# Kernel optimization log

Measured on AMD Instinct MI355X. Metric: run time of the kernel, lower is better.

## Reference

```python
import jax, jax.numpy as jnp
import numpy as np

N = 50000
E = 524288
FA = 133
FB = 14
H = 128
DEPTH = 3


def setup_inputs() -> dict:
    key = jax.random.key(0)
    ks = jax.random.split(key, 8)
    atom_features = jax.random.normal(ks[0], (N, FA), dtype=jnp.float32)
    bond_features = jax.random.normal(ks[1], (E, FB), dtype=jnp.float32)
    edge_index = jax.random.randint(ks[2], (2, E), 0, N, dtype=jnp.int64)
    s_init = 1.0 / np.sqrt(FA + FB)
    s_upd = 1.0 / np.sqrt(2 * H)
    s_read = 1.0 / np.sqrt(H)
    W_init = jax.random.uniform(ks[3], (H, FA + FB), jnp.float32, -s_init, s_init)
    b_init = jnp.zeros((H,), jnp.float32)
    W_upd = jax.random.uniform(ks[4], (H, 2 * H), jnp.float32, -s_upd, s_upd)
    b_upd = jnp.zeros((H,), jnp.float32)
    W_read = jax.random.uniform(ks[5], (H, H), jnp.float32, -s_read, s_read)
    b_read = jnp.zeros((H,), jnp.float32)
    return {
        "atom_features": atom_features,
        "bond_features": bond_features,
        "edge_index": edge_index,
        "W_init": W_init, "b_init": b_init,
        "W_upd": W_upd, "b_upd": b_upd,
        "W_read": W_read, "b_read": b_read,
    }


def reference(atom_features, bond_features, edge_index,
              W_init, b_init, W_upd, b_upd, W_read, b_read):
    src = edge_index[0]
    dst = edge_index[1]
    # edge init: concat(atom[src], bond) -> linear -> relu   [E, H]
    init_in = jnp.concatenate([atom_features[src], bond_features], axis=-1)
    h = jax.nn.relu(init_in @ W_init.T + b_init)
    rev = jnp.arange(E, dtype=jnp.int64) ^ 1  # reverse-edge pairing
    for _ in range(DEPTH):
        sum_in = jax.ops.segment_sum(h, dst, num_segments=N)  # [N, H]
        m = sum_in[src] - h[rev]                              # [E, H]
        h = jax.nn.relu(jnp.concatenate([h, m], axis=-1) @ W_upd.T + b_upd)
    atom_embed = jax.ops.segment_sum(h, dst, num_segments=N)  # [N, H]
    atom_embed = jax.nn.relu(atom_embed @ W_read.T + b_read)
    return atom_embed.sum(axis=0)  # [H]
```

## Files before the change

### kernel.cpp

```cpp
#include <hip/hip_runtime.h>
#include <stdint.h>
#include <stddef.h>

#define N_ATOMS 50000
#define N_EDGES 524288
#define FA 133
#define FB 14
#define H 128
#define DEPTH 3
#define KI 160
#define KB 32
#define KR 128
#define SCAN_NB 98

typedef __attribute__((ext_vector_type(8))) __bf16 bf16x8;
typedef __attribute__((ext_vector_type(4))) float f32x4;

__device__ __forceinline__ uint16_t f2bf(float f) {
    uint32_t u = __builtin_bit_cast(uint32_t, f);
    return (uint16_t)((u + 0x7FFFu + ((u >> 16) & 1u)) >> 16);
}
__device__ __forceinline__ float bf2f(uint16_t h) {
    return __builtin_bit_cast(float, (uint32_t)h << 16);
}

__device__ __forceinline__ void async_load16(const uint16_t* g, uint16_t* l) {
    __builtin_amdgcn_global_load_lds(
        (const __attribute__((address_space(1))) uint32_t*)(const void*)g,
        (__attribute__((address_space(3))) uint32_t*)(void*)l,
        16, 0, 0);
}

__global__ void k_weights(const float* __restrict__ Wi_f,
                          const float* __restrict__ Wu_f,
                          const float* __restrict__ Wr_f,
                          uint16_t* __restrict__ Wa,
                          uint16_t* __restrict__ Wb,
                          uint16_t* __restrict__ Wu0,
                          uint16_t* __restrict__ Wu1,
                          uint16_t* __restrict__ Wu1n,
                          uint16_t* __restrict__ Wr) {
    const int O0 = H * KI, O1 = O0 + H * KB, O2 = O1 + H * 128,
              O3 = O2 + H * 128, O4 = O3 + H * 128, O5 = O4 + H * KR;
    int i = blockIdx.x * 256 + threadIdx.x;
    if (i < O0) {
        int o = i / KI, k = i - o * KI;
        Wa[i] = f2bf((k < FA) ? Wi_f[o * (FA + FB) + k] : 0.f);
    } else if (i < O1) {
        int j = i - O0;
        int o = j >> 5, k = j & 31;
        Wb[j] = f2bf((k < FB) ? Wi_f[o * (FA + FB) + FA + k] : 0.f);
    } else if (i < O2) {
        int j = i - O1;
        int o = j >> 7, k = j & 127;
        Wu0[j] = f2bf(Wu_f[o * 256 + k]);
    } else if (i < O3) {
        int j = i - O2;
        int o = j >> 7, k = j & 127;
        Wu1[j] = f2bf(Wu_f[o * 256 + 128 + k]);
    } else if (i < O4) {
        int j = i - O3;
        int o = j >> 7, k = j & 127;
        Wu1n[j] = f2bf(-Wu_f[o * 256 + 128 + k]);
    } else if (i < O5) {
        int j = i - O4;
        Wr[j] = f2bf(Wr_f[j]);
    }
}

__global__ void k_hist(const int* __restrict__ dstv, int* __restrict__ counts) {
    int e = blockIdx.x * 256 + threadIdx.x;
    if (e < N_EDGES) atomicAdd(&counts[dstv[e]], 1);
}

__global__ void k_scan1(const int* __restrict__ counts,
                        int* __restrict__ lscan, int* __restrict__ partials) {
    __shared__ int s[512];
    const int t = threadIdx.x, b = blockIdx.x;
    const int i = b * 512 + t;
    const int c = (i < N_ATOMS) ? counts[i] : 0;
    s[t] = c;
    __syncthreads();
    for (int off = 1; off < 512; off <<= 1) {
        int u = (t >= off) ? s[t - off] : 0;
        __syncthreads();
        s[t] += u;
        __syncthreads();
    }
    lscan[i] = s[t] - c;
    if (t == 511) partials[b] = s[511];
}

__global__ void k_scan2(const int* __restrict__ partials, int* __restrict__ poff) {
    __shared__ int s[128];
    const int t = threadIdx.x;
    const int v = (t < SCAN_NB) ? partials[t] : 0;
    s[t] = v;
    __syncthreads();
    for (int off = 1; off < 128; off <<= 1) {
        int u = (t >= off) ? s[t - off] : 0;
        __syncthreads();
        s[t] += u;
        __syncthreads();
    }
    poff[t] = s[t] - v;
}

__global__ void k_scan3(const int* __restrict__ lscan, const int* __restrict__ poff,
                        int* __restrict__ row_ptr, int* __restrict__ nxt) {
    const int i = blockIdx.x * 512 + threadIdx.x;
    if (i < N_ATOMS) {
        const int v = poff[blockIdx.x] + lscan[i];
        row_ptr[i] = v;
        nxt[i] = v;
    }
    if (i == 0) row_ptr[N_ATOMS] = N_EDGES;
}

__global__ void k_scatter(const int* __restrict__ dstv, int* __restrict__ nxt,
                          int* __restrict__ edge_slot) {
    int e = blockIdx.x * 256 + threadIdx.x;
    if (e < N_EDGES) {
        int pos = atomicAdd(&nxt[dstv[e]], 1);
        edge_slot[pos] = e;
    }
}

__global__ __launch_bounds__(256, 3) void k_atom_gemm(
    const float* __restrict__ atom, const uint16_t* __restrict__ Wa,
    uint16_t* __restrict__ P) {
    __shared__ __align__(16) uint16_t A[128 * 168];
    const int t = threadIdx.x;
    const int base = blockIdx.x * 128;
    if (t < 128) {
        for (int c = FA; c < KI; ++c) A[t * 168 + c] = 0;
    }
    for (int j = 0; j < 67; ++j) {
        int f = j * 256 + t;
        if (f < 128 * FA) {
            int row = f / FA, col = f - row * FA;
            int a = base + row;
            float v = (a < N_ATOMS) ? atom[(size_t)a * FA + col] : 0.f;
            A[row * 168 + col] = f2bf(v);
        }
    }
    __syncthreads();
    const int w = t >> 6, lane = t & 63;
    const int wm = w >> 1, wn = w & 1;
    const int l15 = lane & 15, q = lane >> 4;
    f32x4 acc[4][4];
    const f32x4 z = {0.f, 0.f, 0.f, 0.f};
    for (int i = 0; i < 4; ++i)
        for (int jj = 0; jj < 4; ++jj) acc[i][jj] = z;
#pragma unroll
    for (int ks = 0; ks < 5; ++ks) {
        const int kk = ks * 32 + q * 8;
        bf16x8 a[4], b[4];
#pragma unroll
        for (int i = 0; i < 4; ++i)
            a[i] = *(const bf16x8*)&A[(wm * 64 + i * 16 + l15) * 168 + kk];
#pragma unroll
        for (int jj = 0; jj < 4; ++jj)
            b[jj] = *(const bf16x8*)&Wa[(wn * 64 + jj * 16 + l15) * KI + kk];
#pragma unroll
        for (int i = 0; i < 4; ++i)
#pragma unroll
            for (int jj = 0; jj < 4; ++jj)
                acc[i][jj] = __builtin_amdgcn_mfma_f32_16x16x32_bf16(a[i], b[jj], acc[i][jj], 0, 0, 0);
    }
    __syncthreads();
#pragma unroll
    for (int jj = 0; jj < 4; ++jj) {
        const int col = wn * 64 + jj * 16 + l15;
#pragma unroll
        for (int i = 0; i < 4; ++i)
#pragma unroll
            for (int r = 0; r < 4; ++r) {
                const int row = wm * 64 + i * 16 + q * 4 + r;
                A[row * 136 + col] = f2bf(acc[i][jj][r]);
            }
    }
    __syncthreads();
    for (int j = 0; j < 8; ++j) {
        int c = j * 256 + t;
        int row = c >> 4, kc = c & 15;
        *(bf16x8*)(P + (size_t)(base + row) * H + kc * 8) =
            *(const bf16x8*)&A[row * 136 + kc * 8];
    }
}

__global__ __launch_bounds__(256, 3) void k_edge_init(
    const float* __restrict__ bond, const int* __restrict__ srcv,
    const uint16_t* __restrict__ Wb, const uint16_t* __restrict__ P,
    const float* __restrict__ b_init, uint16_t* __restrict__ h_out) {
    __shared__ __align__(16) uint16_t Pl[128 * 136];
    __shared__ __align__(16) uint16_t Bb[128 * 40];
    __shared__ int src_lds[128];
    const int t = threadIdx.x;
    const int base = blockIdx.x * 128;
    if (t < 128) {
        src_lds[t] = srcv[base + t];
        for (int c = FB; c < KB; ++c) Bb[t * 40 + c] = 0;
    }
    for (int j = 0; j < 7; ++j) {
        int f = j * 256 + t;
        int row = f / FB, col = f - row * FB;
        Bb[row * 40 + col] = f2bf(bond[(size_t)(base + row) * FB + col]);
    }
    __syncthreads();
    for (int j = 0; j < 8; ++j) {
        int task = j * 256 + t;
        int row = task >> 4, seg = task & 15;
        *(bf16x8*)&Pl[row * 136 + seg * 8] =
            *(const bf16x8*)(P + (size_t)src_lds[row] * H + seg * 8);
    }
    const int w = t >> 6, lane = t & 63;
    const int wm = w >> 1, wn = w & 1;
    const int l15 = lane & 15, q = lane >> 4;
    f32x4 acc[4][4];
    const f32x4 z = {0.f, 0.f, 0.f, 0.f};
    for (int i = 0; i < 4; ++i)
        for (int jj = 0; jj < 4; ++jj) acc[i][jj] = z;
    {
        const int kk = q * 8;
        bf16x8 a[4], b[4];
#pragma unroll
        for (int i = 0; i < 4; ++i)
            a[i] = *(const bf16x8*)&Bb[(wm * 64 + i * 16 + l15) * 40 + kk];
#pragma unroll
        for (int jj = 0; jj < 4; ++jj)
            b[jj] = *(const bf16x8*)&Wb[(wn * 64 + jj * 16 + l15) * KB + kk];
#pragma unroll
        for (int i = 0; i < 4; ++i)
#pragma unroll
            for (int jj = 0; jj < 4; ++jj)
                acc[i][jj] = __builtin_amdgcn_mfma_f32_16x16x32_bf16(a[i], b[jj], acc[i][jj], 0, 0, 0);
    }
    __syncthreads();
#pragma unroll
    for (int jj = 0; jj < 4; ++jj) {
        const int col = wn * 64 + jj * 16 + l15;
        const float bias = b_init[col];
#pragma unroll
        for (int i = 0; i < 4; ++i)
#pragma unroll
            for (int r = 0; r < 4; ++r) {
                const int row = wm * 64 + i * 16 + q * 4 + r;
                float v = acc[i][jj][r] + bf2f(Pl[row * 136 + col]) + bias;
                Pl[row * 136 + col] = f2bf(v > 0.f ? v : 0.f);
            }
    }
    __syncthreads();
    for (int j = 0; j < 8; ++j) {
        int c = j * 256 + t;
        int row = c >> 4, kc = c & 15;
        *(bf16x8*)(h_out + (size_t)(base + row) * H + kc * 8) =
            *(const bf16x8*)&Pl[row * 136 + kc * 8];
    }
}

__global__ __launch_bounds__(256, 4) void k_sg(
    const uint16_t* __restrict__ h, const int* __restrict__ row_ptr,
    const int* __restrict__ edge_slot, const uint16_t* __restrict__ Wu1,
    uint16_t* __restrict__ G) {
    __shared__ __align__(16) uint16_t S[128 * 136];
    const int t = threadIdx.x;
    const int base = blockIdx.x * 128;
    const int qw = t >> 4, ql = t & 15;
    for (int s = 0; s < 8; ++s) {
        const int local = qw * 8 + s;
        const int a = base + local;
        float acc[8];
#pragma unroll
        for (int i = 0; i < 8; ++i) acc[i] = 0.f;
        if (a < N_ATOMS) {
            const int s0 = row_ptr[a], s1 = row_ptr[a + 1];
            int e[4];
#pragma unroll
            for (int i = 0; i < 4; ++i)
                e[i] = (s0 + i < s1) ? edge_slot[s0 + i] : -1;
            int p = s0;
            while (p < s1) {
                bf16x8 v[4];
                bool has[4];
#pragma unroll
                for (int i = 0; i < 4; ++i) {
                    has[i] = (p + i < s1);
                    if (has[i]) v[i] = *(const bf16x8*)(h + (size_t)e[i] * H + ql * 8);
                }
#pragma unroll
                for (int i = 0; i < 4; ++i) {
                    int np = p + 4 + i;
                    e[i] = (np < s1) ? edge_slot[np] : -1;
                }
#pragma unroll
                for (int i = 0; i < 4; ++i)
                    if (has[i]) {
#pragma unroll
                        for (int k = 0; k < 8; ++k) acc[k] += (float)v[i][k];
                    }
                p += 4;
            }
        }
        uint4 o;
        o.x = (uint32_t)f2bf(acc[0]) | ((uint32_t)f2bf(acc[1]) << 16);
        o.y = (uint32_t)f2bf(acc[2]) | ((uint32_t)f2bf(acc[3]) << 16);
        o.z = (uint32_t)f2bf(acc[4]) | ((uint32_t)f2bf(acc[5]) << 16);
        o.w = (uint32_t)f2bf(acc[6]) | ((uint32_t)f2bf(acc[7]) << 16);
        *(uint4*)&S[local * 136 + ql * 8] = o;
    }
    __syncthreads();
    const int w = t >> 6, lane = t & 63;
    const int wm = w >> 1, wn = w & 1;
    const int l15 = lane & 15, q = lane >> 4;
    f32x4 acc[4][4];
    const f32x4 z = {0.f, 0.f, 0.f, 0.f};
    for (int i = 0; i < 4; ++i)
        for (int jj = 0; jj < 4; ++jj) acc[i][jj] = z;
#pragma unroll
    for (int ks = 0; ks < 4; ++ks) {
        const int kk = ks * 32 + q * 8;
        bf16x8 a[4], b[4];
#pragma unroll
        for (int i = 0; i < 4; ++i)
            a[i] = *(const bf16x8*)&S[(wm * 64 + i * 16 + l15) * 136 + kk];
#pragma unroll
        for (int jj = 0; jj < 4; ++jj)
            b[jj] = *(const bf16x8*)&Wu1[(wn * 64 + jj * 16 + l15) * 128 + kk];
#pragma unroll
        for (int i = 0; i < 4; ++i)
#pragma unroll
            for (int jj = 0; jj < 4; ++jj)
                acc[i][jj] = __builtin_amdgcn_mfma_f32_16x16x32_bf16(a[i], b[jj], acc[i][jj], 0, 0, 0);
    }
    __syncthreads();
#pragma unroll
    for (int jj = 0; jj < 4; ++jj) {
        const int col = wn * 64 + jj * 16 + l15;
#pragma unroll
        for (int i = 0; i < 4; ++i)
#pragma unroll
            for (int r = 0; r < 4; ++r) {
                const int row = wm * 64 + i * 16 + q * 4 + r;
                S[row * 136 + col] = f2bf(acc[i][jj][r]);
            }
    }
    __syncthreads();
    for (int j = 0; j < 8; ++j) {
        int c = j * 256 + t;
        int row = c >> 4, kc = c & 15;
        int a_idx = base + row;
        if (a_idx < N_ATOMS)
            *(bf16x8*)(G + (size_t)a_idx * H + kc * 8) =
                *(const bf16x8*)&S[row * 136 + kc * 8];
    }
}

__global__ __launch_bounds__(512, 2) void k_update(
    uint16_t* __restrict__ h_io, const uint16_t* __restrict__ G,
    const int* __restrict__ srcv, const uint16_t* __restrict__ Wu0,
    const uint16_t* __restrict__ Wu1n, const float* __restrict__ b_upd) {
    __shared__ __align__(16) uint16_t A[128 * 128];
    __shared__ __align__(16) uint16_t Gl[128 * 128];
    __shared__ float bias_lds[128];
    const int t = threadIdx.x;
    const int base = blockIdx.x * 128;
    const int w = t >> 6, lane = t & 63;
    if (t < 128) bias_lds[t] = b_upd[t];
#pragma unroll
    for (int j = 0; j < 4; ++j) {
        const int task = j * 512 + t;
        const int row = task >> 4, sp = task & 15;
        const int sl = sp ^ (row & 15);
        const int wavebase = j * 512 + w * 64;
        async_load16(h_io + (size_t)(base + row) * H + sl * 8, A + wavebase * 8);
        const int s = srcv[base + row];
        async_load16(G + (size_t)s * H + sp * 8, Gl + wavebase * 8);
    }
    __syncthreads();
    const int wm = w >> 2, wn = w & 3;
    const int l15 = lane & 15, q = lane >> 4;
    const int l15r = l15 ^ 1;
    f32x4 acc[4][2];
    const f32x4 z = {0.f, 0.f, 0.f, 0.f};
    for (int i = 0; i < 4; ++i)
        for (int jj = 0; jj < 2; ++jj) acc[i][jj] = z;
#pragma unroll
    for (int ks = 0; ks < 4; ++ks) {
        const int ck = ks * 4 + q;
        const int kk = ck * 8;
        bf16x8 a[4], b[2];
#pragma unroll
        for (int i = 0; i < 4; ++i)
            a[i] = *(const bf16x8*)&A[(wm * 64 + i * 16 + l15) * 128 + (ck ^ l15) * 8];
#pragma unroll
        for (int jj = 0; jj < 2; ++jj)
            b[jj] = *(const bf16x8*)&Wu0[(wn * 32 + jj * 16 + l15) * 128 + kk];
#pragma unroll
        for (int i = 0; i < 4; ++i)
#pragma unroll
            for (int jj = 0; jj < 2; ++jj)
                acc[i][jj] = __builtin_amdgcn_mfma_f32_16x16x32_bf16(a[i], b[jj], acc[i][jj], 0, 0, 0);
    }
#pragma unroll
    for (int ks = 0; ks < 4; ++ks) {
        const int ck = ks * 4 + q;
        const int kk = ck * 8;
        bf16x8 a[4], b[2];
#pragma unroll
        for (int i = 0; i < 4; ++i)
            a[i] = *(const bf16x8*)&A[(wm * 64 + i * 16 + l15r) * 128 + (ck ^ l15r) * 8];
#pragma unroll
        for (int jj = 0; jj < 2; ++jj)
            b[jj] = *(const bf16x8*)&Wu1n[(wn * 32 + jj * 16 + l15) * 128 + kk];
#pragma unroll
        for (int i = 0; i < 4; ++i)
#pragma unroll
            for (int jj = 0; jj < 2; ++jj)
                acc[i][jj] = __builtin_amdgcn_mfma_f32_16x16x32_bf16(a[i], b[jj], acc[i][jj], 0, 0, 0);
    }
    __syncthreads();
#pragma unroll
    for (int jj = 0; jj < 2; ++jj) {
        const int col = wn * 32 + jj * 16 + l15;
        const int cc = col >> 3, c7 = col & 7;
#pragma unroll
        for (int i = 0; i < 4; ++i)
#pragma unroll
            for (int r = 0; r < 4; ++r) {
                const int row = wm * 64 + i * 16 + q * 4 + r;
                A[row * 128 + (cc ^ (row & 15)) * 8 + c7] = f2bf(acc[i][jj][r]);
            }
    }
    __syncthreads();
#pragma unroll
    for (int j = 0; j < 4; ++j) {
        const int task = j * 512 + t;
        const int row = task >> 4, sl = task & 15;
        const bf16x8 a8 = *(const bf16x8*)&A[row * 128 + (sl ^ (row & 15)) * 8];
        const bf16x8 g8 = *(const bf16x8*)&Gl[row * 128 + sl * 8];
        uint4 pck;
        uint32_t parts[4];
#pragma unroll
        for (int hw = 0; hw < 4; ++hw) {
            float v0 = (float)a8[hw * 2] + (float)g8[hw * 2] + bias_lds[sl * 8 + hw * 2];
            float v1 = (float)a8[hw * 2 + 1] + (float)g8[hw * 2 + 1] + bias_lds[sl * 8 + hw * 2 + 1];
            v0 = v0 > 0.f ? v0 : 0.f;
            v1 = v1 > 0.f ? v1 : 0.f;
            parts[hw] = (uint32_t)f2bf(v0) | ((uint32_t)f2bf(v1) << 16);
        }
        pck.x = parts[0]; pck.y = parts[1]; pck.z = parts[2]; pck.w = parts[3];
        *(uint4*)(h_io + (size_t)(base + row) * H + sl * 8) = pck;
    }
}

__global__ __launch_bounds__(256, 4) void k_sr(
    const uint16_t* __restrict__ h, const int* __restrict__ row_ptr,
    const int* __restrict__ edge_slot, const uint16_t* __restrict__ Wr,
    const float* __restrict__ b_read, float* __restrict__ out) {
    __shared__ __align__(16) uint16_t S[128 * 136];
    __shared__ float col_lds[128];
    const int t = threadIdx.x;
    const int base = blockIdx.x * 128;
    const int qw = t >> 4, ql = t & 15;
    if (t < 128) col_lds[t] = 0.f;
    for (int s = 0; s < 8; ++s) {
        const int local = qw * 8 + s;
        const int a = base + local;
        float acc[8];
#pragma unroll
        for (int i = 0; i < 8; ++i) acc[i] = 0.f;
        if (a < N_ATOMS) {
            const int s0 = row_ptr[a], s1 = row_ptr[a + 1];
            int e[4];
#pragma unroll
            for (int i = 0; i < 4; ++i)
                e[i] = (s0 + i < s1) ? edge_slot[s0 + i] : -1;
            int p = s0;
            while (p < s1) {
                bf16x8 v[4];
                bool has[4];
#pragma unroll
                for (int i = 0; i < 4; ++i) {
                    has[i] = (p + i < s1);
                    if (has[i]) v[i] = *(const bf16x8*)(h + (size_t)e[i] * H + ql * 8);
                }
#pragma unroll
                for (int i = 0; i < 4; ++i) {
                    int np = p + 4 + i;
                    e[i] = (np < s1) ? edge_slot[np] : -1;
                }
#pragma unroll
                for (int i = 0; i < 4; ++i)
                    if (has[i]) {
#pragma unroll
                        for (int k = 0; k < 8; ++k) acc[k] += (float)v[i][k];
                    }
                p += 4;
            }
        }
        uint4 o;
        o.x = (uint32_t)f2bf(acc[0]) | ((uint32_t)f2bf(acc[1]) << 16);
        o.y = (uint32_t)f2bf(acc[2]) | ((uint32_t)f2bf(acc[3]) << 16);
        o.z = (uint32_t)f2bf(acc[4]) | ((uint32_t)f2bf(acc[5]) << 16);
        o.w = (uint32_t)f2bf(acc[6]) | ((uint32_t)f2bf(acc[7]) << 16);
        *(uint4*)&S[local * 136 + ql * 8] = o;
    }
    __syncthreads();
    const int w = t >> 6, lane = t & 63;
    const int wm = w >> 1, wn = w & 1;
    const int l15 = lane & 15, q = lane >> 4;
    f32x4 acc[4][4];
    const f32x4 z = {0.f, 0.f, 0.f, 0.f};
    for (int i = 0; i < 4; ++i)
        for (int jj = 0; jj < 4; ++jj) acc[i][jj] = z;
#pragma unroll
    for (int ks = 0; ks < 4; ++ks) {
        const int kk = ks * 32 + q * 8;
        bf16x8 a[4], b[4];
#pragma unroll
        for (int i = 0; i < 4; ++i)
            a[i] = *(const bf16x8*)&S[(wm * 64 + i * 16 + l15) * 136 + kk];
#pragma unroll
        for (int jj = 0; jj < 4; ++jj)
            b[jj] = *(const bf16x8*)&Wr[(wn * 64 + jj * 16 + l15) * KR + kk];
#pragma unroll
        for (int i = 0; i < 4; ++i)
#pragma unroll
            for (int jj = 0; jj < 4; ++jj)
                acc[i][jj] = __builtin_amdgcn_mfma_f32_16x16x32_bf16(a[i], b[jj], acc[i][jj], 0, 0, 0);
    }
#pragma unroll
    for (int jj = 0; jj < 4; ++jj) {
        const int col = wn * 64 + jj * 16 + l15;
        const float bias = b_read[col];
        float s = 0.f;
#pragma unroll
        for (int i = 0; i < 4; ++i)
#pragma unroll
            for (int r = 0; r < 4; ++r) {
                const int a_idx = base + wm * 64 + i * 16 + q * 4 + r;
                if (a_idx < N_ATOMS) {
                    float v = acc[i][jj][r] + bias;
                    s += (v > 0.f) ? v : 0.f;
                }
            }
        atomicAdd(&col_lds[col], s);
    }
    __syncthreads();
    if (t < 128) atomicAdd(&out[t], col_lds[t]);
}

extern "C" void kernel_launch(void* const* d_in, const int* in_sizes, int n_in,
                              void* d_out, int out_size, void* d_ws, size_t ws_size,
                              hipStream_t stream) {
    (void)in_sizes; (void)n_in; (void)out_size; (void)ws_size;
    const float* atom   = (const float*)d_in[0];
    const float* bond   = (const float*)d_in[1];
    const int* edge_idx = (const int*)d_in[2];
    const float* W_init = (const float*)d_in[3];
    const float* b_init = (const float*)d_in[4];
    const float* W_upd  = (const float*)d_in[5];
    const float* b_upd  = (const float*)d_in[6];
    const float* W_read = (const float*)d_in[7];
    const float* b_read = (const float*)d_in[8];
    float* out = (float*)d_out;

    char* ws = (char*)d_ws;
    constexpr size_t SZ_H    = (size_t)N_EDGES * H * 2;
    constexpr size_t OFF_H   = 0;
    constexpr size_t OFF_P   = OFF_H + SZ_H;
    constexpr size_t OFF_G   = OFF_P + (size_t)N_ATOMS * H * 2;
    constexpr size_t OFF_WA  = OFF_G + (size_t)N_ATOMS * H * 2;
    constexpr size_t OFF_WB  = OFF_WA + (size_t)H * KI * 2;
    constexpr size_t OFF_WU0 = OFF_WB + (size_t)H * KB * 2;
    constexpr size_t OFF_WU1 = OFF_WU0 + (size_t)H * 128 * 2;
    constexpr size_t OFF_WU1N= OFF_WU1 + (size_t)H * 128 * 2;
    constexpr size_t OFF_WR  = OFF_WU1N + (size_t)H * 128 * 2;
    constexpr size_t OFF_CNT = OFF_WR + (size_t)H * KR * 2;
    constexpr size_t OFF_RP  = OFF_CNT + 200192;
    constexpr size_t OFF_NXT = OFF_RP + 200704;
    constexpr size_t OFF_ES  = OFF_NXT + 200192;
    constexpr size_t OFF_LS  = OFF_ES + (size_t)N_EDGES * 4;
    constexpr size_t OFF_PT  = OFF_LS + 512 * SCAN_NB * 4;
    constexpr size_t OFF_PO  = OFF_PT + 512;

    uint16_t* h     = (uint16_t*)(ws + OFF_H);
    uint16_t* P     = (uint16_t*)(ws + OFF_P);
    uint16_t* G     = (uint16_t*)(ws + OFF_G);
    uint16_t* Wa    = (uint16_t*)(ws + OFF_WA);
    uint16_t* Wb    = (uint16_t*)(ws + OFF_WB);
    uint16_t* Wu0   = (uint16_t*)(ws + OFF_WU0);
    uint16_t* Wu1   = (uint16_t*)(ws + OFF_WU1);
    uint16_t* Wu1n  = (uint16_t*)(ws + OFF_WU1N);
    uint16_t* Wr    = (uint16_t*)(ws + OFF_WR);
    int* counts     = (int*)(ws + OFF_CNT);
    int* row_ptr    = (int*)(ws + OFF_RP);
    int* nxt        = (int*)(ws + OFF_NXT);
    int* edge_slot  = (int*)(ws + OFF_ES);
    int* lscan      = (int*)(ws + OFF_LS);
    int* partials   = (int*)(ws + OFF_PT);
    int* poff       = (int*)(ws + OFF_PO);

    const int* srcv = edge_idx;
    const int* dstv = edge_idx + N_EDGES;

    hipMemsetAsync(counts, 0, N_ATOMS * sizeof(int), stream);
    hipMemsetAsync(d_out, 0, H * sizeof(float), stream);

    const int NW = H * KI + H * KB + 3 * H * 128 + H * KR;
    k_weights<<<(NW + 255) / 256, 256, 0, stream>>>(
        W_init, W_upd, W_read, Wa, Wb, Wu0, Wu1, Wu1n, Wr);
    k_hist<<<(N_EDGES + 255) / 256, 256, 0, stream>>>(dstv, counts);
    k_scan1<<<SCAN_NB, 512, 0, stream>>>(counts, lscan, partials);
    k_scan2<<<1, 128, 0, stream>>>(partials, poff);
    k_scan3<<<SCAN_NB, 512, 0, stream>>>(lscan, poff, row_ptr, nxt);
    k_scatter<<<(N_EDGES + 255) / 256, 256, 0, stream>>>(dstv, nxt, edge_slot);

    k_atom_gemm<<<(N_ATOMS + 127) / 128, 256, 0, stream>>>(atom, Wa, P);
    k_edge_init<<<N_EDGES / 128, 256, 0, stream>>>(bond, srcv, Wb, P, b_init, h);

    for (int d = 0; d < DEPTH; ++d) {
        k_sg<<<(N_ATOMS + 127) / 128, 256, 0, stream>>>(h, row_ptr, edge_slot, Wu1, G);
        k_update<<<N_EDGES / 128, 512, 0, stream>>>(h, G, srcv, Wu0, Wu1n, b_upd);
    }
    k_sr<<<(N_ATOMS + 127) / 128, 256, 0, stream>>>(h, row_ptr, edge_slot, Wr, b_read, out);
}
```

Measured before the change: 675.2 us.

## Rework edge init with async gathers, widen gather unroll, use packed bf16 convert

Rewrites k_edge_init to run 512 threads per block and to gather the projected atom rows with global_load_lds async copies, overlapping them with bond staging. The MFMA result goes to a separate LDS tile and is combined with the gathered rows in a vectorized epilogue. The segment-sum gathers in k_sg and k_sr prefetch 8 neighbours instead of 4, which raises memory-level parallelism at the cost of more registers. Float-to-bf16 packing uses the hardware packed convert builtin when it is available.

```diff
diff --git a/kernel.cpp b/kernel.cpp
--- a/kernel.cpp
+++ b/kernel.cpp
@@ -22,6 +22,15 @@
 }
 __device__ __forceinline__ float bf2f(uint16_t h) {
     return __builtin_bit_cast(float, (uint32_t)h << 16);
+}
+__device__ __forceinline__ uint32_t pack2(float a, float b) {
+#if __has_builtin(__builtin_amdgcn_cvt_pk_bf16_f32)
+    typedef __attribute__((ext_vector_type(2))) __bf16 bf16x2_t;
+    bf16x2_t v = __builtin_amdgcn_cvt_pk_bf16_f32(a, b);
+    return __builtin_bit_cast(uint32_t, v);
+#else
+    return (uint32_t)f2bf(a) | ((uint32_t)f2bf(b) << 16);
+#endif
 }
 
 __device__ __forceinline__ void async_load16(const uint16_t* g, uint16_t* l) {
@@ -189,73 +198,84 @@
     }
 }
 
-__global__ __launch_bounds__(256, 3) void k_edge_init(
+__global__ __launch_bounds__(512, 2) void k_edge_init(
     const float* __restrict__ bond, const int* __restrict__ srcv,
     const uint16_t* __restrict__ Wb, const uint16_t* __restrict__ P,
     const float* __restrict__ b_init, uint16_t* __restrict__ h_out) {
-    __shared__ __align__(16) uint16_t Pl[128 * 136];
+    __shared__ __align__(16) uint16_t Pl[128 * 128];
+    __shared__ __align__(16) uint16_t Pk[128 * 136];
     __shared__ __align__(16) uint16_t Bb[128 * 40];
-    __shared__ int src_lds[128];
+    __shared__ float bias_lds[128];
     const int t = threadIdx.x;
     const int base = blockIdx.x * 128;
-    if (t < 128) {
-        src_lds[t] = srcv[base + t];
-        for (int c = FB; c < KB; ++c) Bb[t * 40 + c] = 0;
-    }
-    for (int j = 0; j < 7; ++j) {
-        int f = j * 256 + t;
-        int row = f / FB, col = f - row * FB;
-        Bb[row * 40 + col] = f2bf(bond[(size_t)(base + row) * FB + col]);
-    }
-    __syncthreads();
+    const int w = t >> 6, lane = t & 63;
+    if (t < 128) bias_lds[t] = b_init[t];
+#pragma unroll
+    for (int j = 0; j < 4; ++j) {
+        const int task = j * 512 + t;
+        const int row = task >> 4, sp = task & 15;
+        const int wavebase = j * 512 + w * 64;
+        const int s = srcv[base + row];
+        async_load16(P + (size_t)s * H + sp * 8, Pl + wavebase * 8);
+    }
+#pragma unroll
     for (int j = 0; j < 8; ++j) {
-        int task = j * 256 + t;
-        int row = task >> 4, seg = task & 15;
-        *(bf16x8*)&Pl[row * 136 + seg * 8] =
-            *(const bf16x8*)(P + (size_t)src_lds[row] * H + seg * 8);
-    }
-    const int w = t >> 6, lane = t & 63;
-    const int wm = w >> 1, wn = w & 1;
+        const int task = j * 512 + t;
+        const int row = task >> 5, col = task & 31;
+        float v = (col < FB) ? bond[(size_t)(base + row) * FB + col] : 0.f;
+        Bb[row * 40 + col] = f2bf(v);
+    }
+    __syncthreads();
+    const int wm = w >> 2, wn = w & 3;
     const int l15 = lane & 15, q = lane >> 4;
-    f32x4 acc[4][4];
+    f32x4 acc[4][2];
     const f32x4 z = {0.f, 0.f, 0.f, 0.f};
     for (int i = 0; i < 4; ++i)
-        for (int jj = 0; jj < 4; ++jj) acc[i][jj] = z;
+        for (int jj = 0; jj < 2; ++jj) acc[i][jj] = z;
     {
-        const int kk = q * 8;
-        bf16x8 a[4], b[4];
-#pragma unroll
-        for (int i = 0; i < 4; ++i)
-            a[i] = *(const bf16x8*)&Bb[(wm * 64 + i * 16 + l15) * 40 + kk];
-#pragma unroll
-        for (int jj = 0; jj < 4; ++jj)
-            b[jj] = *(const bf16x8*)&Wb[(wn * 64 + jj * 16 + l15) * KB + kk];
-#pragma unroll
-        for (int i = 0; i < 4; ++i)
-#pragma unroll
-            for (int jj = 0; jj < 4; ++jj)
+        bf16x8 a[4], b[2];
+#pragma unroll
+        for (int i = 0; i < 4; ++i)
+            a[i] = *(const bf16x8*)&Bb[(wm * 64 + i * 16 + l15) * 40 + q * 8];
+#pragma unroll
+        for (int jj = 0; jj < 2; ++jj)
+            b[jj] = *(const bf16x8*)&Wb[(wn * 32 + jj * 16 + l15) * KB + q * 8];
+#pragma unroll
+        for (int i = 0; i < 4; ++i)
+#pragma unroll
+            for (int jj = 0; jj < 2; ++jj)
                 acc[i][jj] = __builtin_amdgcn_mfma_f32_16x16x32_bf16(a[i], b[jj], acc[i][jj], 0, 0, 0);
     }
-    __syncthreads();
-#pragma unroll
-    for (int jj = 0; jj < 4; ++jj) {
-        const int col = wn * 64 + jj * 16 + l15;
-        const float bias = b_init[col];
+#pragma unroll
+    for (int jj = 0; jj < 2; ++jj) {
+        const int col = wn * 32 + jj * 16 + l15;
 #pragma unroll
         for (int i = 0; i < 4; ++i)
 #pragma unroll
             for (int r = 0; r < 4; ++r) {
                 const int row = wm * 64 + i * 16 + q * 4 + r;
-                float v = acc[i][jj][r] + bf2f(Pl[row * 136 + col]) + bias;
-                Pl[row * 136 + col] = f2bf(v > 0.f ? v : 0.f);
+                Pk[row * 136 + col] = f2bf(acc[i][jj][r]);
             }
     }
     __syncthreads();
-    for (int j = 0; j < 8; ++j) {
-        int c = j * 256 + t;
-        int row = c >> 4, kc = c & 15;
-        *(bf16x8*)(h_out + (size_t)(base + row) * H + kc * 8) =
-            *(const bf16x8*)&Pl[row * 136 + kc * 8];
+#pragma unroll
+    for (int j = 0; j < 4; ++j) {
+        const int task = j * 512 + t;
+        const int row = task >> 4, sl = task & 15;
+        const bf16x8 a8 = *(const bf16x8*)&Pk[row * 136 + sl * 8];
+        const bf16x8 p8 = *(const bf16x8*)&Pl[row * 128 + sl * 8];
+        uint4 pck;
+        uint32_t parts[4];
+#pragma unroll
+        for (int hw = 0; hw < 4; ++hw) {
+            float v0 = (float)a8[hw * 2] + (float)p8[hw * 2] + bias_lds[sl * 8 + hw * 2];
+            float v1 = (float)a8[hw * 2 + 1] + (float)p8[hw * 2 + 1] + bias_lds[sl * 8 + hw * 2 + 1];
+            v0 = v0 > 0.f ? v0 : 0.f;
+            v1 = v1 > 0.f ? v1 : 0.f;
+            parts[hw] = pack2(v0, v1);
+        }
+        pck.x = parts[0]; pck.y = parts[1]; pck.z = parts[2]; pck.w = parts[3];
+        *(uint4*)(h_out + (size_t)(base + row) * H + sl * 8) = pck;
     }
 }
 
@@ -275,38 +295,38 @@
         for (int i = 0; i < 8; ++i) acc[i] = 0.f;
         if (a < N_ATOMS) {
             const int s0 = row_ptr[a], s1 = row_ptr[a + 1];
-            int e[4];
-#pragma unroll
-            for (int i = 0; i < 4; ++i)
+            int e[8];
+#pragma unroll
+            for (int i = 0; i < 8; ++i)
                 e[i] = (s0 + i < s1) ? edge_slot[s0 + i] : -1;
             int p = s0;
             while (p < s1) {
-                bf16x8 v[4];
-                bool has[4];
-#pragma unroll
-                for (int i = 0; i < 4; ++i) {
+                bf16x8 v[8];
+                bool has[8];
+#pragma unroll
+                for (int i = 0; i < 8; ++i) {
                     has[i] = (p + i < s1);
                     if (has[i]) v[i] = *(const bf16x8*)(h + (size_t)e[i] * H + ql * 8);
                 }
 #pragma unroll
-                for (int i = 0; i < 4; ++i) {
-                    int np = p + 4 + i;
+                for (int i = 0; i < 8; ++i) {
+                    int np = p + 8 + i;
                     e[i] = (np < s1) ? edge_slot[np] : -1;
                 }
 #pragma unroll
-                for (int i = 0; i < 4; ++i)
+                for (int i = 0; i < 8; ++i)
                     if (has[i]) {
 #pragma unroll
                         for (int k = 0; k < 8; ++k) acc[k] += (float)v[i][k];
                     }
-                p += 4;
+                p += 8;
             }
         }
         uint4 o;
-        o.x = (uint32_t)f2bf(acc[0]) | ((uint32_t)f2bf(acc[1]) << 16);
-        o.y = (uint32_t)f2bf(acc[2]) | ((uint32_t)f2bf(acc[3]) << 16);
-        o.z = (uint32_t)f2bf(acc[4]) | ((uint32_t)f2bf(acc[5]) << 16);
-        o.w = (uint32_t)f2bf(acc[6]) | ((uint32_t)f2bf(acc[7]) << 16);
+        o.x = pack2(acc[0], acc[1]);
+        o.y = pack2(acc[2], acc[3]);
+        o.z = pack2(acc[4], acc[5]);
+        o.w = pack2(acc[6], acc[7]);
         *(uint4*)&S[local * 136 + ql * 8] = o;
     }
     __syncthreads();
@@ -447,7 +467,7 @@
             float v1 = (float)a8[hw * 2 + 1] + (float)g8[hw * 2 + 1] + bias_lds[sl * 8 + hw * 2 + 1];
             v0 = v0 > 0.f ? v0 : 0.f;
             v1 = v1 > 0.f ? v1 : 0.f;
-            parts[hw] = (uint32_t)f2bf(v0) | ((uint32_t)f2bf(v1) << 16);
+            parts[hw] = pack2(v0, v1);
         }
         pck.x = parts[0]; pck.y = parts[1]; pck.z = parts[2]; pck.w = parts[3];
         *(uint4*)(h_io + (size_t)(base + row) * H + sl * 8) = pck;
@@ -472,38 +492,38 @@
         for (int i = 0; i < 8; ++i) acc[i] = 0.f;
         if (a < N_ATOMS) {
             const int s0 = row_ptr[a], s1 = row_ptr[a + 1];
-            int e[4];
-#pragma unroll
-            for (int i = 0; i < 4; ++i)
+            int e[8];
+#pragma unroll
+            for (int i = 0; i < 8; ++i)
                 e[i] = (s0 + i < s1) ? edge_slot[s0 + i] : -1;
             int p = s0;
             while (p < s1) {
-                bf16x8 v[4];
-                bool has[4];
-#pragma unroll
-                for (int i = 0; i < 4; ++i) {
+                bf16x8 v[8];
+                bool has[8];
+#pragma unroll
+                for (int i = 0; i < 8; ++i) {
                     has[i] = (p + i < s1);
                     if (has[i]) v[i] = *(const bf16x8*)(h + (size_t)e[i] * H + ql * 8);
                 }
 #pragma unroll
-                for (int i = 0; i < 4; ++i) {
-                    int np = p + 4 + i;
+                for (int i = 0; i < 8; ++i) {
+                    int np = p + 8 + i;
                     e[i] = (np < s1) ? edge_slot[np] : -1;
                 }
 #pragma unroll
-                for (int i = 0; i < 4; ++i)
+                for (int i = 0; i < 8; ++i)
                     if (has[i]) {
 #pragma unroll
                         for (int k = 0; k < 8; ++k) acc[k] += (float)v[i][k];
                     }
-                p += 4;
+                p += 8;
             }
         }
         uint4 o;
-        o.x = (uint32_t)f2bf(acc[0]) | ((uint32_t)f2bf(acc[1]) << 16);
-        o.y = (uint32_t)f2bf(acc[2]) | ((uint32_t)f2bf(acc[3]) << 16);
-        o.z = (uint32_t)f2bf(acc[4]) | ((uint32_t)f2bf(acc[5]) << 16);
-        o.w = (uint32_t)f2bf(acc[6]) | ((uint32_t)f2bf(acc[7]) << 16);
+        o.x = pack2(acc[0], acc[1]);
+        o.y = pack2(acc[2], acc[3]);
+        o.z = pack2(acc[4], acc[5]);
+        o.w = pack2(acc[6], acc[7]);
         *(uint4*)&S[local * 136 + ql * 8] = o;
     }
     __syncthreads();
@@ -618,7 +638,7 @@
     k_scatter<<<(N_EDGES + 255) / 256, 256, 0, stream>>>(dstv, nxt, edge_slot);
 
     k_atom_gemm<<<(N_ATOMS + 127) / 128, 256, 0, stream>>>(atom, Wa, P);
-    k_edge_init<<<N_EDGES / 128, 256, 0, stream>>>(bond, srcv, Wb, P, b_init, h);
+    k_edge_init<<<N_EDGES / 128, 512, 0, stream>>>(bond, srcv, Wb, P, b_init, h);
 
     for (int d = 0; d < DEPTH; ++d) {
         k_sg<<<(N_ATOMS + 127) / 128, 256, 0, stream>>>(h, row_ptr, edge_slot, Wu1, G);
```

After: 693.7 us. 1.03x slower.
